# Performance work log

Hardware: AMD Instinct MI355X
Metric: run time of the kernel (lower is better)

The kernel has to match this reference:

```python
import jax, jax.numpy as jnp
import numpy as np

S, B, E, H, R, NCLS = 128, 512, 128, 256, 1024, 10
FB = 1.0  # forget_bias


def setup_inputs() -> dict:
    key = jax.random.key(0)
    ks = jax.random.split(key, 8)
    s = lambda *d: 1.0 / np.sqrt(d[-1])
    x = jax.random.normal(ks[0], (S, B, E), dtype=jnp.float32)
    W = jax.random.normal(ks[1], (4 * H, E), dtype=jnp.float32) * s(E)
    U = jax.random.normal(ks[2], (4 * H, H), dtype=jnp.float32) * s(H)
    b = jnp.zeros((4 * H,), dtype=jnp.float32)
    W1 = jax.random.normal(ks[3], (R, S * H), dtype=jnp.float32) * s(S * H)
    b1 = jnp.zeros((R,), dtype=jnp.float32)
    W2 = jax.random.normal(ks[4], (NCLS, R), dtype=jnp.float32) * s(R)
    b2 = jnp.zeros((NCLS,), dtype=jnp.float32)
    return {"x": x, "W": W, "U": U, "b": b, "W1": W1, "b1": b1, "W2": W2, "b2": b2}


def _urlstm(x, W, U, b):
    # x: [S,B,E] time-major. Returns per-step hidden states [S,B,H].
    xg = jnp.einsum('sbe,ge->sbg', x, W) + b  # precompute input contribution [S,B,4H]

    def step(carry, xg_t):
        h, c = carry
        gates = xg_t + h @ U.T  # [B,4H]
        f_, r_, u_, o_ = jnp.split(gates, 4, axis=-1)
        f = jax.nn.sigmoid(f_ + FB)
        r = jax.nn.sigmoid(r_ - FB)
        g = 2.0 * r * f + (1.0 - 2.0 * r) * f * f
        c = g * c + (1.0 - g) * jnp.tanh(u_)
        h = jax.nn.sigmoid(o_) * jnp.tanh(c)
        return (h, c), h

    h0 = jnp.zeros((x.shape[1], H), dtype=x.dtype)
    c0 = jnp.zeros((x.shape[1], H), dtype=x.dtype)
    _, hs = jax.lax.scan(step, (h0, c0), xg)
    return hs


def reference(x, W, U, b, W1, b1, W2, b2):
    hs = _urlstm(x, W, U, b)                      # [S,B,H]
    y = hs.transpose(1, 0, 2).reshape(B, S * H)   # [B, S*H]
    y = jax.nn.relu(y @ W1.T + b1)                # [B,R]
    return y @ W2.T + b2                          # [B,10]
```

## Files before the change

kernel.cpp:

```cpp
#include <hip/hip_runtime.h>
#include <hip/hip_fp16.h>

#define S_ 128
#define Bt_ 512
#define E_ 128
#define H_ 256
#define G_ 1024
#define SH_ 32768
#define SEG_ 32
#define NSEG_ 4

typedef _Float16 half8 __attribute__((ext_vector_type(8)));
typedef _Float16 h2 __attribute__((ext_vector_type(2)));
typedef float f32x4 __attribute__((ext_vector_type(4)));

__device__ __forceinline__ float dot2(unsigned int w, unsigned int h, float acc) {
#if __has_builtin(__builtin_amdgcn_fdot2)
  return __builtin_amdgcn_fdot2(__builtin_bit_cast(h2, w), __builtin_bit_cast(h2, h), acc, false);
#else
  __half2 wh = __builtin_bit_cast(__half2, w);
  __half2 hx = __builtin_bit_cast(__half2, h);
  acc = fmaf(__half2float(wh.x), __half2float(hx.x), acc);
  acc = fmaf(__half2float(wh.y), __half2float(hx.y), acc);
  return acc;
#endif
}

__device__ __forceinline__ float sigm(float x) { return 1.0f / (1.0f + __expf(-x)); }
__device__ __forceinline__ float tanh_f(float x) { return 1.0f - 2.0f / (__expf(2.0f * x) + 1.0f); }

__global__ void k_conv_u(const float* __restrict__ U, unsigned int* __restrict__ up) {
  int idx = blockIdx.x * 256 + threadIdx.x;
  int kp = idx >> 10, g = idx & 1023;
  __half2 v;
  v.x = __float2half(U[g * H_ + 2 * kp]);
  v.y = __float2half(U[g * H_ + 2 * kp + 1]);
  up[idx] = __builtin_bit_cast(unsigned int, v);
}

__global__ void k_conv_w(const float* __restrict__ W, __half* __restrict__ Wg) {
  int idx = blockIdx.x * 256 + threadIdx.x;
  Wg[idx] = __float2half(W[idx]);
}

__global__ __launch_bounds__(256) void k_xg(const float* __restrict__ x,
                                            const __half* __restrict__ Wg,
                                            const float* __restrict__ bias,
                                            __half* __restrict__ xg) {
  __shared__ __half As[128][72];
  __shared__ __half Bs[128][72];
  const int t = threadIdx.x;
  const int n0 = blockIdx.x * 128;
  const int m0 = blockIdx.y * 128;
  const int w = t >> 6, l = t & 63;
  const int l15 = l & 15, l4 = l >> 4;
  const int wm = (w >> 1) * 64, wn = (w & 1) * 64;
  const int r = t >> 1, hf = t & 1;

  f32x4 acc[4][4];
#pragma unroll
  for (int i = 0; i < 4; ++i)
#pragma unroll
    for (int j = 0; j < 4; ++j) acc[i][j] = (f32x4)0.0f;

#pragma unroll
  for (int kt = 0; kt < 2; ++kt) {
    {
      const float* xrow = x + (size_t)(m0 + r) * E_ + kt * 64 + hf * 32;
#pragma unroll
      for (int q = 0; q < 4; ++q) {
        float4 v0 = *(const float4*)(xrow + q * 8);
        float4 v1 = *(const float4*)(xrow + q * 8 + 4);
        __half2 p0, p1, p2, p3;
        p0.x = __float2half(v0.x); p0.y = __float2half(v0.y);
        p1.x = __float2half(v0.z); p1.y = __float2half(v0.w);
        p2.x = __float2half(v1.x); p2.y = __float2half(v1.y);
        p3.x = __float2half(v1.z); p3.y = __float2half(v1.w);
        uint4 pk;
        pk.x = __builtin_bit_cast(unsigned int, p0);
        pk.y = __builtin_bit_cast(unsigned int, p1);
        pk.z = __builtin_bit_cast(unsigned int, p2);
        pk.w = __builtin_bit_cast(unsigned int, p3);
        *(uint4*)&As[r][hf * 32 + q * 8] = pk;
      }
      const __half* brow = Wg + (size_t)(n0 + r) * E_ + kt * 64 + hf * 32;
#pragma unroll
      for (int q = 0; q < 4; ++q) {
        uint4 v = *(const uint4*)(brow + q * 8);
        *(uint4*)&Bs[r][hf * 32 + q * 8] = v;
      }
    }
    __syncthreads();
#pragma unroll
    for (int kk = 0; kk < 2; ++kk) {
      half8 af[4], bf[4];
#pragma unroll
      for (int i = 0; i < 4; ++i) af[i] = *(const half8*)&As[wm + i * 16 + l15][kk * 32 + l4 * 8];
#pragma unroll
      for (int j = 0; j < 4; ++j) bf[j] = *(const half8*)&Bs[wn + j * 16 + l15][kk * 32 + l4 * 8];
#pragma unroll
      for (int i = 0; i < 4; ++i)
#pragma unroll
        for (int j = 0; j < 4; ++j)
          acc[i][j] = __builtin_amdgcn_mfma_f32_16x16x32_f16(af[i], bf[j], acc[i][j], 0, 0, 0);
    }
    __syncthreads();
  }

#pragma unroll
  for (int j = 0; j < 4; ++j) {
    int col = n0 + wn + j * 16 + l15;
    float bv = bias[col];
#pragma unroll
    for (int i = 0; i < 4; ++i) {
      int mrow = m0 + wm + i * 16 + l4 * 4;
#pragma unroll
      for (int rg = 0; rg < 4; ++rg)
        xg[(size_t)(mrow + rg) * G_ + col] = __float2half(acc[i][j][rg] + bv);
    }
  }
}

__global__ __launch_bounds__(256, 1) void k_rec_seg(const __half* __restrict__ xg,
                                                    const unsigned int* __restrict__ up,
                                                    __half* __restrict__ hs,
                                                    float* __restrict__ c_state,
                                                    __half* __restrict__ h_state,
                                                    int s0) {
  __shared__ float gsh[4][2][256];
  __shared__ unsigned int hh[256];
  const int t = threadIdx.x;
  const int w = t >> 6, l = t & 63;
  const int b0 = blockIdx.x * 2;
  const int j = t;
  const int rbias = (blockIdx.x * 5) & 127;

  float c_reg[2];
  __half hcur[2];
#pragma unroll
  for (int eb = 0; eb < 2; ++eb) {
    c_reg[eb] = (s0 == 0) ? 0.0f : c_state[(b0 + eb) * H_ + j];
    hcur[eb] = (s0 == 0) ? __float2half(0.0f) : h_state[(b0 + eb) * H_ + j];
    ((__half*)hh)[((j >> 1) * 2 + eb) * 2 + (j & 1)] = hcur[eb];
  }

  const unsigned int* uw = up + w * 256 + l * 4;

  asm volatile("s_waitcnt lgkmcnt(0)" ::: "memory");
  __builtin_amdgcn_s_barrier();

  for (int sl = 0; sl < SEG_; ++sl) {
    const int s = s0 + sl;

    uint2 xv[2];
#pragma unroll
    for (int eb = 0; eb < 2; ++eb)
      xv[eb] = *(const uint2*)(xg + ((size_t)sl * Bt_ + b0 + eb) * G_ + w * 256 + l * 4);
    float acc[2][4];
#pragma unroll
    for (int eb = 0; eb < 2; ++eb) {
      __half2 a01 = __builtin_bit_cast(__half2, xv[eb].x);
      __half2 a23 = __builtin_bit_cast(__half2, xv[eb].y);
      acc[eb][0] = __half2float(a01.x);
      acc[eb][1] = __half2float(a01.y);
      acc[eb][2] = __half2float(a23.x);
      acc[eb][3] = __half2float(a23.y);
    }

#pragma unroll 32
    for (int i = 0; i < 128; ++i) {
      const int kp = (i + rbias) & 127;
      uint4 wv = *(const uint4*)(uw + (size_t)kp * G_);
      uint2 hv = *(const uint2*)&hh[kp * 2];
      acc[0][0] = dot2(wv.x, hv.x, acc[0][0]);
      acc[0][1] = dot2(wv.y, hv.x, acc[0][1]);
      acc[0][2] = dot2(wv.z, hv.x, acc[0][2]);
      acc[0][3] = dot2(wv.w, hv.x, acc[0][3]);
      acc[1][0] = dot2(wv.x, hv.y, acc[1][0]);
      acc[1][1] = dot2(wv.y, hv.y, acc[1][1]);
      acc[1][2] = dot2(wv.z, hv.y, acc[1][2]);
      acc[1][3] = dot2(wv.w, hv.y, acc[1][3]);
    }

#pragma unroll
    for (int eb = 0; eb < 2; ++eb) {
      float4 fv = {acc[eb][0], acc[eb][1], acc[eb][2], acc[eb][3]};
      *(float4*)&gsh[w][eb][l * 4] = fv;
    }
    asm volatile("s_waitcnt lgkmcnt(0)" ::: "memory");
    __builtin_amdgcn_s_barrier();

#pragma unroll
    for (int eb = 0; eb < 2; ++eb) {
      float f_ = gsh[0][eb][j];
      float r_ = gsh[1][eb][j];
      float u_ = gsh[2][eb][j];
      float o_ = gsh[3][eb][j];
      float f = sigm(f_ + 1.0f);
      float r = sigm(r_ - 1.0f);
      float g = 2.0f * r * f + (1.0f - 2.0f * r) * f * f;
      c_reg[eb] = g * c_reg[eb] + (1.0f - g) * tanh_f(u_);
      float hn = tanh_f(c_reg[eb]) * sigm(o_);
      hcur[eb] = __float2half(hn);
      ((__half*)hh)[((j >> 1) * 2 + eb) * 2 + (j & 1)] = hcur[eb];
      hs[(size_t)(b0 + eb) * SH_ + s * H_ + j] = hcur[eb];
    }
    asm volatile("s_waitcnt lgkmcnt(0)" ::: "memory");
    __builtin_amdgcn_s_barrier();
  }

#pragma unroll
  for (int eb = 0; eb < 2; ++eb) {
    c_state[(b0 + eb) * H_ + j] = c_reg[eb];
    h_state[(b0 + eb) * H_ + j] = hcur[eb];
  }
}

__global__ __launch_bounds__(256) void k_gemm1(const __half* __restrict__ hs,
                                               const float* __restrict__ W1,
                                               float* __restrict__ part) {
  __shared__ __half As[128][40];
  __shared__ __half Bs[64][40];
  const int t = threadIdx.x;
  const int n0 = blockIdx.x * 64;
  const int m0 = blockIdx.y * 128;
  const int kz = blockIdx.z;
  const int w = t >> 6, l = t & 63;
  const int l15 = l & 15, l4 = l >> 4;
  const int wm = (w >> 1) * 64;
  const int wn = (w & 1) * 32;
  const int ra = t >> 1, ca = (t & 1) * 16;
  const int rb = t >> 2, cb = (t & 3) * 8;

  f32x4 acc[4][2];
#pragma unroll
  for (int i = 0; i < 4; ++i)
#pragma unroll
    for (int j = 0; j < 2; ++j) acc[i][j] = (f32x4)0.0f;

  const size_t a_base = (size_t)(m0 + ra) * SH_ + (size_t)kz * 4096 + ca;
  const size_t b_base = (size_t)(n0 + rb) * SH_ + (size_t)kz * 4096 + cb;

  for (int kt = 0; kt < 128; ++kt) {
    uint4 av0 = *(const uint4*)(hs + a_base + kt * 32);
    uint4 av1 = *(const uint4*)(hs + a_base + kt * 32 + 8);
    float4 bv0 = *(const float4*)(W1 + b_base + kt * 32);
    float4 bv1 = *(const float4*)(W1 + b_base + kt * 32 + 4);
    __syncthreads();
    *(uint4*)&As[ra][ca] = av0;
    *(uint4*)&As[ra][ca + 8] = av1;
    {
      __half2 p0, p1, p2, p3;
      p0.x = __float2half(bv0.x); p0.y = __float2half(bv0.y);
      p1.x = __float2half(bv0.z); p1.y = __float2half(bv0.w);
      p2.x = __float2half(bv1.x); p2.y = __float2half(bv1.y);
      p3.x = __float2half(bv1.z); p3.y = __float2half(bv1.w);
      uint4 pk;
      pk.x = __builtin_bit_cast(unsigned int, p0);
      pk.y = __builtin_bit_cast(unsigned int, p1);
      pk.z = __builtin_bit_cast(unsigned int, p2);
      pk.w = __builtin_bit_cast(unsigned int, p3);
      *(uint4*)&Bs[rb][cb] = pk;
    }
    __syncthreads();
    half8 af[4], bf[2];
#pragma unroll
    for (int i = 0; i < 4; ++i) af[i] = *(const half8*)&As[wm + i * 16 + l15][l4 * 8];
#pragma unroll
    for (int j = 0; j < 2; ++j) bf[j] = *(const half8*)&Bs[wn + j * 16 + l15][l4 * 8];
#pragma unroll
    for (int i = 0; i < 4; ++i)
#pragma unroll
      for (int j = 0; j < 2; ++j)
        acc[i][j] = __builtin_amdgcn_mfma_f32_16x16x32_f16(af[i], bf[j], acc[i][j], 0, 0, 0);
  }

#pragma unroll
  for (int i = 0; i < 4; ++i)
#pragma unroll
    for (int j = 0; j < 2; ++j) {
      int col = n0 + wn + j * 16 + l15;
      int mrow = m0 + wm + i * 16 + l4 * 4;
#pragma unroll
      for (int rg = 0; rg < 4; ++rg)
        part[(size_t)kz * 524288 + (size_t)(mrow + rg) * G_ + col] = acc[i][j][rg];
    }
}

__global__ void k_reduce(const float* __restrict__ part, const float* __restrict__ b1,
                         __half* __restrict__ y) {
  int flat = blockIdx.x * 256 + threadIdx.x;
  int n = flat & 1023;
  float s = b1[n];
#pragma unroll
  for (int z = 0; z < 8; ++z) s += part[(size_t)z * 524288 + flat];
  y[flat] = __float2half(fmaxf(s, 0.0f));
}

__global__ void k_head(const __half* __restrict__ y, const float* __restrict__ W2,
                       const float* __restrict__ b2, float* __restrict__ out) {
  const int b = blockIdx.x;
  const int lane = threadIdx.x;
  float yv[16];
#pragma unroll
  for (int i = 0; i < 16; ++i) yv[i] = __half2float(y[(size_t)b * 1024 + i * 64 + lane]);
  for (int n = 0; n < 10; ++n) {
    float p = 0.0f;
#pragma unroll
    for (int i = 0; i < 16; ++i) p += yv[i] * W2[n * 1024 + i * 64 + lane];
#pragma unroll
    for (int off = 32; off > 0; off >>= 1) p += __shfl_down(p, off);
    if (lane == 0) out[b * 10 + n] = p + b2[n];
  }
}

extern "C" void kernel_launch(void* const* d_in, const int* in_sizes, int n_in,
                              void* d_out, int out_size, void* d_ws, size_t ws_size,
                              hipStream_t stream) {
  const float* x  = (const float*)d_in[0];
  const float* W  = (const float*)d_in[1];
  const float* U  = (const float*)d_in[2];
  const float* b  = (const float*)d_in[3];
  const float* W1 = (const float*)d_in[4];
  const float* b1 = (const float*)d_in[5];
  const float* W2 = (const float*)d_in[6];
  const float* b2 = (const float*)d_in[7];
  float* out = (float*)d_out;

  char* base = (char*)d_ws;
  __half*       hs      = (__half*)(base);
  __half*       xg      = (__half*)(base + 33554432);
  float*        part    = (float*)(base + 67108864);
  __half*       y       = (__half*)(base + 83886080);
  unsigned int* up      = (unsigned int*)(base + 84934656);
  __half*       Wg      = (__half*)(base + 85458944);
  float*        c_state = (float*)(base + 85721088);
  __half*       h_state = (__half*)(base + 86245376);

  k_conv_u<<<512, 256, 0, stream>>>(U, up);
  k_conv_w<<<512, 256, 0, stream>>>(W, Wg);

  for (int sg = 0; sg < NSEG_; ++sg) {
    const float* xseg = x + (size_t)sg * SEG_ * Bt_ * E_;
    k_xg<<<dim3(8, SEG_ * Bt_ / 128), 256, 0, stream>>>(xseg, Wg, b, xg);
    k_rec_seg<<<256, 256, 0, stream>>>(xg, up, hs, c_state, h_state, sg * SEG_);
  }

  k_gemm1<<<dim3(16, 4, 8), 256, 0, stream>>>(hs, W1, part);
  k_reduce<<<2048, 256, 0, stream>>>(part, b1, y);
  k_head<<<512, 64, 0, stream>>>(y, W2, b2, out);
}
```

Baseline: 1.060 ms.

## Software-pipeline recurrent weight loads with inline asm and manual vmcnt waits

Replaces the compiler-scheduled loop over recurrent weight rows with a hand-pipelined loop. Weight rows are fetched with inline-asm global_load_dwordx4 into a 4-deep ring of register buffers, keeping three groups of 8 loads in flight ahead of the dot2 compute, with explicit s_waitcnt vmcnt counts and sched_barriers. The aim is to hide global/L2 latency on the per-timestep weight stream, which sits on the serial critical path. In exchange it holds about 128 extra VGPRs for the buffers, which can lower occupancy, and correctness depends on the hand-written vmcnt bookkeeping staying in step with the issued loads.

```diff
diff --git a/kernel.cpp b/kernel.cpp
--- a/kernel.cpp
+++ b/kernel.cpp
@@ -154,8 +154,23 @@
 
     uint2 xv[2];
 #pragma unroll
-    for (int eb = 0; eb < 2; ++eb)
-      xv[eb] = *(const uint2*)(xg + ((size_t)sl * Bt_ + b0 + eb) * G_ + w * 256 + l * 4);
+    for (int eb = 0; eb < 2; ++eb) {
+      const __half* xp = xg + ((size_t)sl * Bt_ + b0 + eb) * G_ + w * 256 + l * 4;
+      asm volatile("global_load_dwordx2 %0, %1, off" : "=v"(xv[eb]) : "v"(xp) : "memory");
+    }
+
+    uint4 buf[4][8];
+#pragma unroll
+    for (int pg = 0; pg < 3; ++pg)
+#pragma unroll
+      for (int r = 0; r < 8; ++r) {
+        const int kp = ((pg * 8 + r) + rbias) & 127;
+        const unsigned int* p = uw + (size_t)kp * G_;
+        asm volatile("global_load_dwordx4 %0, %1, off" : "=v"(buf[pg][r]) : "v"(p) : "memory");
+      }
+
+    asm volatile("s_waitcnt vmcnt(24)" ::: "memory");
+    __builtin_amdgcn_sched_barrier(0);
     float acc[2][4];
 #pragma unroll
     for (int eb = 0; eb < 2; ++eb) {
@@ -167,19 +182,37 @@
       acc[eb][3] = __half2float(a23.y);
     }
 
-#pragma unroll 32
-    for (int i = 0; i < 128; ++i) {
-      const int kp = (i + rbias) & 127;
-      uint4 wv = *(const uint4*)(uw + (size_t)kp * G_);
-      uint2 hv = *(const uint2*)&hh[kp * 2];
-      acc[0][0] = dot2(wv.x, hv.x, acc[0][0]);
-      acc[0][1] = dot2(wv.y, hv.x, acc[0][1]);
-      acc[0][2] = dot2(wv.z, hv.x, acc[0][2]);
-      acc[0][3] = dot2(wv.w, hv.x, acc[0][3]);
-      acc[1][0] = dot2(wv.x, hv.y, acc[1][0]);
-      acc[1][1] = dot2(wv.y, hv.y, acc[1][1]);
-      acc[1][2] = dot2(wv.z, hv.y, acc[1][2]);
-      acc[1][3] = dot2(wv.w, hv.y, acc[1][3]);
+#pragma unroll
+    for (int g = 0; g < 16; ++g) {
+      if (g + 3 < 16) {
+#pragma unroll
+        for (int r = 0; r < 8; ++r) {
+          const int kp = (((g + 3) * 8 + r) + rbias) & 127;
+          const unsigned int* p = uw + (size_t)kp * G_;
+          asm volatile("global_load_dwordx4 %0, %1, off"
+                       : "=v"(buf[(g + 3) & 3][r]) : "v"(p) : "memory");
+        }
+      }
+      if (g + 3 < 16)      asm volatile("s_waitcnt vmcnt(24)" ::: "memory");
+      else if (g == 13)    asm volatile("s_waitcnt vmcnt(16)" ::: "memory");
+      else if (g == 14)    asm volatile("s_waitcnt vmcnt(8)" ::: "memory");
+      else                 asm volatile("s_waitcnt vmcnt(0)" ::: "memory");
+      __builtin_amdgcn_sched_barrier(0);
+
+#pragma unroll
+      for (int r = 0; r < 8; ++r) {
+        const int kp = ((g * 8 + r) + rbias) & 127;
+        uint4 wv = buf[g & 3][r];
+        uint2 hv = *(const uint2*)&hh[kp * 2];
+        acc[0][0] = dot2(wv.x, hv.x, acc[0][0]);
+        acc[0][1] = dot2(wv.y, hv.x, acc[0][1]);
+        acc[0][2] = dot2(wv.z, hv.x, acc[0][2]);
+        acc[0][3] = dot2(wv.w, hv.x, acc[0][3]);
+        acc[1][0] = dot2(wv.x, hv.y, acc[1][0]);
+        acc[1][1] = dot2(wv.y, hv.y, acc[1][1]);
+        acc[1][2] = dot2(wv.z, hv.y, acc[1][2]);
+        acc[1][3] = dot2(wv.w, hv.y, acc[1][3]);
+      }
     }
 
 #pragma unroll
```

Result: slower. 1.247 ms (+17.6%).
